# Performance work log

Measured on AMD Instinct MI355X. Metric: run time of the kernel, lower is better.

The kernel has to match this reference:

```python
import jax, jax.numpy as jnp
import numpy as np

EBD_DIM = 32
N_PARTS = 17
B, P, H, W = 16, 20, 128, 128


def _gather_vecs(ebds, kpts):
    # ebds: [17*D, H, W]; kpts: [P, 17, 2] normalized coords in [0,1)
    D = EBD_DIM
    flat = ebds.reshape(N_PARTS, D, H * W).transpose(0, 2, 1)  # [17, HW, D]
    ys = jnp.floor(kpts[..., 0] * H).astype(jnp.int32)          # [P, 17]
    xs = jnp.floor(kpts[..., 1] * W).astype(jnp.int32)          # [P, 17]
    lin = ys * W + xs                                           # [P, 17]
    k = jnp.arange(N_PARTS)[None, :]                            # [1, 17] part index
    return flat[k, lin]                                         # [P, 17, D]


def setup_inputs() -> dict:
    key = jax.random.key(0)
    k1, k2 = jax.random.split(key)
    ebd_batch = jax.random.normal(k1, (B, N_PARTS * EBD_DIM, H, W), dtype=jnp.float32)
    kpts = jax.random.uniform(k2, (B, P, N_PARTS, 2), dtype=jnp.float32)
    return {"ebd_batch": ebd_batch, "kpts": kpts}


def reference(ebd_batch, kpts):
    # Gather per-keypoint embedding vectors: [B, P, 17, D]
    vecs = jax.vmap(_gather_vecs)(ebd_batch, kpts)
    # Per-person mean embedding (segment mean over the 17 keypoints): [B, P, D]
    means = vecs.mean(axis=2)
    # Pull: per person, mean |vec - person_mean| (elementwise abs, matching
    # the original sqrt(x**2)), summed over people -> [B]
    pull = jnp.abs(vecs - means[:, :, None, :]).mean(axis=(2, 3)).sum(axis=1)
    # Push: mean pairwise |mean_p - mean_q| over P x P pairs and D dims -> [B]
    push = jnp.abs(means[:, :, None, :] - means[:, None, :, :]).mean(axis=(1, 2, 3))
    return (push.mean() + pull.mean()) / 2
```

## Files before the change

### kernel.cpp

```cpp
#include <hip/hip_runtime.h>
#include <math.h>

#define BB 16
#define PP 20
#define NPARTS 17
#define DD 32
#define HH 128
#define WW 128
#define HWN (HH*WW)
#define CC (NPARTS*DD)

__device__ __forceinline__ float block_sum_256(float v, float* wsum) {
    #pragma unroll
    for (int off = 32; off > 0; off >>= 1) v += __shfl_down(v, off);
    int lane = threadIdx.x & 63;
    int wid  = threadIdx.x >> 6;
    if (lane == 0) wsum[wid] = v;
    __syncthreads();
    float t = 0.f;
    if (threadIdx.x == 0) t = wsum[0] + wsum[1] + wsum[2] + wsum[3];
    return t;
}

__global__ __launch_bounds__(256) void k1_gather_pull(
        const float* __restrict__ ebd, const float* __restrict__ kpts,
        float* __restrict__ means, float* __restrict__ pull_pp,
        unsigned int* __restrict__ counter) {
    const int bp  = blockIdx.x;
    const int b   = bp / PP;
    const int tid = threadIdx.x;

    if (bp == 0 && tid == 0) *counter = 0u;

    __shared__ float vec[CC];
    __shared__ int   lin[NPARTS];
    __shared__ float mean_s[DD];
    __shared__ float wsum[4];

    if (tid < NPARTS) {
        float ky = kpts[(bp * NPARTS + tid) * 2 + 0];
        float kx = kpts[(bp * NPARTS + tid) * 2 + 1];
        int y = (int)floorf(ky * (float)HH);
        int x = (int)floorf(kx * (float)WW);
        y = min(max(y, 0), HH - 1);
        x = min(max(x, 0), WW - 1);
        lin[tid] = y * WW + x;
    }
    __syncthreads();

    const float* base = ebd + (size_t)b * CC * HWN;
    for (int i = tid; i < CC; i += 256) {
        int k = i >> 5;
        vec[i] = base[(size_t)i * HWN + lin[k]];
    }
    __syncthreads();

    if (tid < DD) {
        float s = 0.f;
        #pragma unroll
        for (int k = 0; k < NPARTS; ++k) s += vec[k * DD + tid];
        float m = s * (1.0f / (float)NPARTS);
        mean_s[tid] = m;
        means[bp * DD + tid] = m;
    }
    __syncthreads();

    float ps = 0.f;
    for (int i = tid; i < CC; i += 256)
        ps += fabsf(vec[i] - mean_s[i & (DD - 1)]);

    float tot = block_sum_256(ps, wsum);
    if (tid == 0) pull_pp[bp] = tot * (1.0f / (float)CC);
}

__global__ __launch_bounds__(256) void k2_push_final(
        const float* __restrict__ means, const float* __restrict__ pull_pp,
        float* __restrict__ partial_b, unsigned int* __restrict__ counter,
        float* __restrict__ out) {
    const int b   = blockIdx.x;
    const int tid = threadIdx.x;

    __shared__ float m[PP * DD];
    __shared__ float wsum[4];

    for (int i = tid; i < PP * DD; i += 256)
        m[i] = means[b * PP * DD + i];
    __syncthreads();

    float acc = 0.f;
    if (tid < PP * (DD / 4)) {
        int p  = tid >> 3;
        int d4 = tid & 7;
        float4 mp = *reinterpret_cast<const float4*>(&m[p * DD + d4 * 4]);
        #pragma unroll
        for (int q = 0; q < PP; ++q) {
            float4 mq = *reinterpret_cast<const float4*>(&m[q * DD + d4 * 4]);
            acc += fabsf(mp.x - mq.x) + fabsf(mp.y - mq.y)
                 + fabsf(mp.z - mq.z) + fabsf(mp.w - mq.w);
        }
    }
    float v = acc * (1.0f / (float)(PP * PP * DD));
    if (tid < PP) v += pull_pp[b * PP + tid];

    float tot = block_sum_256(v, wsum);

    if (tid == 0) {
        __hip_atomic_store(&partial_b[b], tot, __ATOMIC_RELEASE,
                           __HIP_MEMORY_SCOPE_AGENT);
        unsigned int old = __hip_atomic_fetch_add(counter, 1u, __ATOMIC_ACQ_REL,
                                                  __HIP_MEMORY_SCOPE_AGENT);
        if (old == BB - 1) {
            float s = 0.f;
            #pragma unroll
            for (int i = 0; i < BB; ++i)
                s += __hip_atomic_load(&partial_b[i], __ATOMIC_ACQUIRE,
                                       __HIP_MEMORY_SCOPE_AGENT);
            out[0] = s * (1.0f / (2.0f * (float)BB));
        }
    }
}

extern "C" void kernel_launch(void* const* d_in, const int* in_sizes, int n_in,
                              void* d_out, int out_size, void* d_ws, size_t ws_size,
                              hipStream_t stream) {
    const float* ebd  = (const float*)d_in[0];
    const float* kpts = (const float*)d_in[1];
    float* out = (float*)d_out;

    float* ws            = (float*)d_ws;
    float* means         = ws;
    float* pull_pp       = means + BB * PP * DD;
    float* partial_b     = pull_pp + BB * PP;
    unsigned int* counter = (unsigned int*)(partial_b + BB);

    k1_gather_pull<<<BB * PP, 256, 0, stream>>>(ebd, kpts, means, pull_pp, counter);
    k2_push_final<<<BB, 256, 0, stream>>>(means, pull_pp, partial_b, counter, out);
}
```

Baseline: 16.11 us.

## Fuse gather/pull and push kernels via per-batch last-block atomic counter

```diff
diff --git a/kernel.cpp b/kernel.cpp
--- a/kernel.cpp
+++ b/kernel.cpp
@@ -3,113 +3,111 @@
 
 #define BB 16
 #define PP 20
-#define NPARTS 17
+#define NP 17
 #define DD 32
 #define HH 128
 #define WW 128
 #define HWN (HH*WW)
-#define CC (NPARTS*DD)
+#define CC (NP*DD)
 
 __device__ __forceinline__ float block_sum_256(float v, float* wsum) {
     #pragma unroll
     for (int off = 32; off > 0; off >>= 1) v += __shfl_down(v, off);
-    int lane = threadIdx.x & 63;
-    int wid  = threadIdx.x >> 6;
-    if (lane == 0) wsum[wid] = v;
+    if ((threadIdx.x & 63) == 0) wsum[threadIdx.x >> 6] = v;
     __syncthreads();
     float t = 0.f;
     if (threadIdx.x == 0) t = wsum[0] + wsum[1] + wsum[2] + wsum[3];
     return t;
 }
 
-__global__ __launch_bounds__(256) void k1_gather_pull(
+__global__ __launch_bounds__(256) void ae_fused(
         const float* __restrict__ ebd, const float* __restrict__ kpts,
         float* __restrict__ means, float* __restrict__ pull_pp,
-        unsigned int* __restrict__ counter) {
+        float* __restrict__ partial_b, unsigned int* __restrict__ bcnt,
+        unsigned int* __restrict__ fcnt, float* __restrict__ out) {
     const int bp  = blockIdx.x;
     const int b   = bp / PP;
     const int tid = threadIdx.x;
 
-    if (bp == 0 && tid == 0) *counter = 0u;
-
-    __shared__ float vec[CC];
-    __shared__ int   lin[NPARTS];
+    __shared__ float vec_t[CC];
+    __shared__ int   lin_s[NP];
     __shared__ float mean_s[DD];
     __shared__ float wsum[4];
+    __shared__ int   flag;
+    __shared__ float msh[PP * DD];
 
-    if (tid < NPARTS) {
-        float ky = kpts[(bp * NPARTS + tid) * 2 + 0];
-        float kx = kpts[(bp * NPARTS + tid) * 2 + 1];
-        int y = (int)floorf(ky * (float)HH);
-        int x = (int)floorf(kx * (float)WW);
-        y = min(max(y, 0), HH - 1);
-        x = min(max(x, 0), WW - 1);
-        lin[tid] = y * WW + x;
+    if (tid < NP) {
+        float2 kv = reinterpret_cast<const float2*>(kpts)[bp * NP + tid];
+        int y = min(max((int)floorf(kv.x * (float)HH), 0), HH - 1);
+        int x = min(max((int)floorf(kv.y * (float)WW), 0), WW - 1);
+        lin_s[tid] = y * WW + x;
     }
     __syncthreads();
 
     const float* base = ebd + (size_t)b * CC * HWN;
-    for (int i = tid; i < CC; i += 256) {
-        int k = i >> 5;
-        vec[i] = base[(size_t)i * HWN + lin[k]];
+    #pragma unroll 3
+    for (int j = tid; j < CC; j += 256) {
+        int d = j / NP;
+        int k = j - d * NP;
+        vec_t[j] = base[(size_t)(k * DD + d) * HWN + lin_s[k]];
     }
     __syncthreads();
 
     if (tid < DD) {
         float s = 0.f;
         #pragma unroll
-        for (int k = 0; k < NPARTS; ++k) s += vec[k * DD + tid];
-        float m = s * (1.0f / (float)NPARTS);
+        for (int k = 0; k < NP; ++k) s += vec_t[tid * NP + k];
+        float m = s * (1.0f / (float)NP);
         mean_s[tid] = m;
         means[bp * DD + tid] = m;
     }
     __syncthreads();
 
     float ps = 0.f;
-    for (int i = tid; i < CC; i += 256)
-        ps += fabsf(vec[i] - mean_s[i & (DD - 1)]);
+    #pragma unroll 3
+    for (int j = tid; j < CC; j += 256)
+        ps += fabsf(vec_t[j] - mean_s[j / NP]);
 
     float tot = block_sum_256(ps, wsum);
-    if (tid == 0) pull_pp[bp] = tot * (1.0f / (float)CC);
-}
-
-__global__ __launch_bounds__(256) void k2_push_final(
-        const float* __restrict__ means, const float* __restrict__ pull_pp,
-        float* __restrict__ partial_b, unsigned int* __restrict__ counter,
-        float* __restrict__ out) {
-    const int b   = blockIdx.x;
-    const int tid = threadIdx.x;
-
-    __shared__ float m[PP * DD];
-    __shared__ float wsum[4];
+    if (tid == 0) {
+        __hip_atomic_store(&pull_pp[bp], tot * (1.0f / (float)CC),
+                           __ATOMIC_RELEASE, __HIP_MEMORY_SCOPE_AGENT);
+        unsigned int old = __hip_atomic_fetch_add(&bcnt[b], 1u, __ATOMIC_ACQ_REL,
+                                                  __HIP_MEMORY_SCOPE_AGENT);
+        flag = (old == PP - 1);
+    }
+    __syncthreads();
+    if (!flag) return;
 
     for (int i = tid; i < PP * DD; i += 256)
-        m[i] = means[b * PP * DD + i];
+        msh[i] = __hip_atomic_load(&means[b * PP * DD + i], __ATOMIC_ACQUIRE,
+                                   __HIP_MEMORY_SCOPE_AGENT);
     __syncthreads();
 
     float acc = 0.f;
     if (tid < PP * (DD / 4)) {
         int p  = tid >> 3;
         int d4 = tid & 7;
-        float4 mp = *reinterpret_cast<const float4*>(&m[p * DD + d4 * 4]);
+        float4 mp = *reinterpret_cast<const float4*>(&msh[p * DD + d4 * 4]);
         #pragma unroll
         for (int q = 0; q < PP; ++q) {
-            float4 mq = *reinterpret_cast<const float4*>(&m[q * DD + d4 * 4]);
+            float4 mq = *reinterpret_cast<const float4*>(&msh[q * DD + d4 * 4]);
             acc += fabsf(mp.x - mq.x) + fabsf(mp.y - mq.y)
                  + fabsf(mp.z - mq.z) + fabsf(mp.w - mq.w);
         }
     }
     float v = acc * (1.0f / (float)(PP * PP * DD));
-    if (tid < PP) v += pull_pp[b * PP + tid];
+    if (tid < PP)
+        v += __hip_atomic_load(&pull_pp[b * PP + tid], __ATOMIC_ACQUIRE,
+                               __HIP_MEMORY_SCOPE_AGENT);
 
-    float tot = block_sum_256(v, wsum);
-
+    float tot2 = block_sum_256(v, wsum);
     if (tid == 0) {
-        __hip_atomic_store(&partial_b[b], tot, __ATOMIC_RELEASE,
+        __hip_atomic_store(&partial_b[b], tot2, __ATOMIC_RELEASE,
                            __HIP_MEMORY_SCOPE_AGENT);
-        unsigned int old = __hip_atomic_fetch_add(counter, 1u, __ATOMIC_ACQ_REL,
-                                                  __HIP_MEMORY_SCOPE_AGENT);
-        if (old == BB - 1) {
+        unsigned int o2 = __hip_atomic_fetch_add(fcnt, 1u, __ATOMIC_ACQ_REL,
+                                                 __HIP_MEMORY_SCOPE_AGENT);
+        if (o2 == BB - 1) {
             float s = 0.f;
             #pragma unroll
             for (int i = 0; i < BB; ++i)
@@ -127,12 +125,14 @@
     const float* kpts = (const float*)d_in[1];
     float* out = (float*)d_out;
 
-    float* ws            = (float*)d_ws;
-    float* means         = ws;
-    float* pull_pp       = means + BB * PP * DD;
-    float* partial_b     = pull_pp + BB * PP;
-    unsigned int* counter = (unsigned int*)(partial_b + BB);
+    float* ws             = (float*)d_ws;
+    float* means          = ws;
+    float* pull_pp        = means + BB * PP * DD;
+    float* partial_b      = pull_pp + BB * PP;
+    unsigned int* bcnt    = (unsigned int*)(partial_b + BB);
+    unsigned int* fcnt    = bcnt + BB;
 
-    k1_gather_pull<<<BB * PP, 256, 0, stream>>>(ebd, kpts, means, pull_pp, counter);
-    k2_push_final<<<BB, 256, 0, stream>>>(means, pull_pp, partial_b, counter, out);
+    hipMemsetAsync(bcnt, 0, (BB + 1) * sizeof(unsigned int), stream);
+    ae_fused<<<BB * PP, 256, 0, stream>>>(ebd, kpts, means, pull_pp,
+                                          partial_b, bcnt, fcnt, out);
 }
```

New measurement: 32.69 us. 2.03x slower.
